# Kernel optimization log

Measured on AMD Instinct MI355X. Metric: run time of the kernel, lower is better.

Reference implementation:

```python
import jax, jax.numpy as jnp
import numpy as np


def setup_inputs() -> dict:
    key = jax.random.key(0)
    # [batch, heads, seq, head_dim]
    hidden_states = jax.random.normal(key, (2, 16, 2048, 64), dtype=jnp.float32)
    return {"hidden_states": hidden_states}


def reference(hidden_states):
    q = k = v = hidden_states
    # scores: [b, h, s, s] -- note: NO 1/sqrt(d) scaling, matching the original.
    scores = jnp.einsum("bhqd,bhkd->bhqk", q, k)
    a = jax.nn.softmax(scores, axis=-1)
    out = jnp.einsum("bhqk,bhkd->bhqd", a, v)
    return out
```

## Files before the change

kernel.cpp:

```cpp
#include <hip/hip_runtime.h>
#include <hip/hip_bf16.h>
#include <stdint.h>


typedef __bf16 bf16x8 __attribute__((ext_vector_type(8)));
typedef __bf16 bf16x4 __attribute__((ext_vector_type(4)));
typedef __bf16 bf16x2 __attribute__((ext_vector_type(2)));
typedef float f32x4 __attribute__((ext_vector_type(4)));
typedef float f32x16 __attribute__((ext_vector_type(16)));
typedef unsigned int u32x4v __attribute__((ext_vector_type(4)));

#define SEQ 2048
#define HD 64
#define KVB 64
#define NBH 32
#define NTILE (SEQ / KVB)
#define IMG_BYTES 8192
#define PAIR_BYTES 16384
#define IMG_TOT ((size_t)NBH * NTILE * PAIR_BYTES)
#define PART_BYTES ((size_t)2 * NBH * SEQ * HD * 4)
#define ML_BYTES ((size_t)2 * NBH * SEQ * 8)
#define WS_IMG IMG_TOT
#define WS_SPLIT (IMG_TOT + PART_BYTES + ML_BYTES)

#define QPB 128

__device__ __forceinline__ int swz(int row, int byteoff) {
    return byteoff ^ ((row & 7) << 4);
}

__device__ __forceinline__ float fexp2(float x) {
    float r;
    asm("v_exp_f32 %0, %1" : "=v"(r) : "v"(x));
    return r;
}

__device__ __forceinline__ unsigned pk_bf16(float a, float b) {
    bf16x2 v;
    v[0] = (__bf16)a;
    v[1] = (__bf16)b;
    return __builtin_bit_cast(unsigned, v);
}

__device__ __forceinline__ bf16x8 read_frag8(const char* base, int r, int p0) {
    const char* rowp = base + r * 128;
    const int rr = r & 15;
    bf16x4 lo = *(const bf16x4*)(rowp + (((p0 + 0) ^ rr) << 3));
    bf16x4 hi4 = *(const bf16x4*)(rowp + (((p0 + 1) ^ rr) << 3));
    bf16x8 f;
    f[0] = lo[0]; f[1] = lo[1]; f[2] = lo[2]; f[3] = lo[3];
    f[4] = hi4[0]; f[5] = hi4[1]; f[6] = hi4[2]; f[7] = hi4[3];
    return f;
}

#if __has_builtin(__builtin_amdgcn_global_load_lds)
#define HAVE_GLLDS 1
typedef const __attribute__((address_space(1))) unsigned int* gas_t;
typedef __attribute__((address_space(3))) unsigned int* las_t;
__device__ __forceinline__ void gl_lds16(const void* g, void* l) {
    __builtin_amdgcn_global_load_lds((gas_t)g, (las_t)l, 16, 0, 0);
}
#else
#define HAVE_GLLDS 0
#endif

__global__ __launch_bounds__(256)
void prep_kernel(const float* __restrict__ x, char* __restrict__ ws) {
    const int bh = blockIdx.y;
    const int tile = blockIdx.x;
    const int kv0 = tile * KVB;
    const int t = threadIdx.x;
    const int srow = t >> 2;
    const int scq = (t & 3) * 16;
    const float* __restrict__ X = x + (size_t)bh * SEQ * HD;
    char* __restrict__ img = ws + ((size_t)bh * NTILE + tile) * PAIR_BYTES;

    const int rr = srow & 15;
    const int p = scq >> 2;

    {
        const float* src = X + (size_t)(kv0 + srow) * HD + scq;
        float4 a = *(const float4*)(src);
        float4 b = *(const float4*)(src + 4);
        float4 c = *(const float4*)(src + 8);
        float4 d = *(const float4*)(src + 12);
        bf16x4 k0, k1, k2, k3;
        k0[0] = (__bf16)a.x; k0[1] = (__bf16)a.y; k0[2] = (__bf16)a.z; k0[3] = (__bf16)a.w;
        k1[0] = (__bf16)b.x; k1[1] = (__bf16)b.y; k1[2] = (__bf16)b.z; k1[3] = (__bf16)b.w;
        k2[0] = (__bf16)c.x; k2[1] = (__bf16)c.y; k2[2] = (__bf16)c.z; k2[3] = (__bf16)c.w;
        k3[0] = (__bf16)d.x; k3[1] = (__bf16)d.y; k3[2] = (__bf16)d.z; k3[3] = (__bf16)d.w;
        char* rowp = img + srow * 128;
        *(bf16x4*)(rowp + (((p + 0) ^ rr) << 3)) = k0;
        *(bf16x4*)(rowp + (((p + 1) ^ rr) << 3)) = k1;
        *(bf16x4*)(rowp + (((p + 2) ^ rr) << 3)) = k2;
        *(bf16x4*)(rowp + (((p + 3) ^ rr) << 3)) = k3;
    }
    {
        bf16x4 g0, g1, g2, g3;
#pragma unroll
        for (int j = 0; j < 4; ++j) {
            g0[j] = (__bf16)X[(size_t)(kv0 + scq + j) * HD + srow];
            g1[j] = (__bf16)X[(size_t)(kv0 + scq + 4 + j) * HD + srow];
            g2[j] = (__bf16)X[(size_t)(kv0 + scq + 8 + j) * HD + srow];
            g3[j] = (__bf16)X[(size_t)(kv0 + scq + 12 + j) * HD + srow];
        }
        char* rowp = img + IMG_BYTES + srow * 128;
        *(bf16x4*)(rowp + (((p + 0) ^ rr) << 3)) = g0;
        *(bf16x4*)(rowp + (((p + 1) ^ rr) << 3)) = g1;
        *(bf16x4*)(rowp + (((p + 2) ^ rr) << 3)) = g2;
        *(bf16x4*)(rowp + (((p + 3) ^ rr) << 3)) = g3;
    }
}

template <int SPLIT>
__global__ __launch_bounds__(256, 4)
void attn_img_kernel(const float* __restrict__ x, const char* __restrict__ ws,
                     float* __restrict__ outp, float* __restrict__ part,
                     float2* __restrict__ ml) {
    __shared__ __align__(16) char kbuf[2][IMG_BYTES];
    __shared__ __align__(16) char vbuf[2][IMG_BYTES];

    const int wg = blockIdx.x;
    const int sid = (wg & 7) * 64 + (wg >> 3);
    const int bh = sid >> 4;
    const int q0 = (sid & 15) * QPB;
    const int half = SPLIT ? blockIdx.y : 0;
    const int tile0 = SPLIT ? half * (NTILE / 2) : 0;
    const int ntiles = SPLIT ? (NTILE / 2) : NTILE;

    const float* __restrict__ X = x + (size_t)bh * SEQ * HD;
    const char* __restrict__ wsb = ws + (size_t)bh * NTILE * PAIR_BYTES;

    const int t = threadIdx.x;
    const int wave = t >> 6;
    const int lane = t & 63;
    const int ln = lane & 31;
    const int hi = lane >> 5;

    const int qbase = q0 + wave * 32;

    const float SCL = 1.4426950408889634f;
    bf16x8 qf[4];
    float m = 0.f;
    {
        const float* qsrc = X + (size_t)(qbase + ln) * HD;
#pragma unroll
        for (int j = 0; j < 16; ++j) {
            float4 v = *(const float4*)(qsrc + j * 4);
            m += v.x * v.x + v.y * v.y + v.z * v.z + v.w * v.w;
        }
        m *= SCL;
#pragma unroll
        for (int dt = 0; dt < 4; ++dt) {
            const float* s8 = qsrc + dt * 16 + hi * 8;
            float4 a = *(const float4*)s8;
            float4 b = *(const float4*)(s8 + 4);
            bf16x8 f;
            f[0] = (__bf16)(a.x * SCL); f[1] = (__bf16)(a.y * SCL);
            f[2] = (__bf16)(a.z * SCL); f[3] = (__bf16)(a.w * SCL);
            f[4] = (__bf16)(b.x * SCL); f[5] = (__bf16)(b.y * SCL);
            f[6] = (__bf16)(b.z * SCL); f[7] = (__bf16)(b.w * SCL);
            qf[dt] = f;
        }
    }

    f32x16 acc0, acc1;
#pragma unroll
    for (int i = 0; i < 16; ++i) { acc0[i] = 0.f; acc1[i] = 0.f; }
    float l = 0.f;

#if HAVE_GLLDS
    {
        char* base = (wave & 2) ? &vbuf[0][(wave & 1) * 4096] : &kbuf[0][(wave & 1) * 4096];
        const char* sp = wsb + (size_t)tile0 * PAIR_BYTES + wave * 4096 + lane * 16;
#pragma unroll
        for (int j = 0; j < 4; ++j)
            gl_lds16(sp + j * 1024, base + j * 1024);
    }
#else
    {
        const char* img = wsb + (size_t)tile0 * PAIR_BYTES;
#pragma unroll
        for (int q = 0; q < 4; ++q) {
            bf16x8 d0 = *(const bf16x8*)(img + q * 4096 + t * 16);
            char* dst = (q & 2) ? &vbuf[0][(q & 1) * 4096] : &kbuf[0][(q & 1) * 4096];
            *(bf16x8*)&dst[t * 16] = d0;
        }
    }
#endif
    __syncthreads();

    for (int it = 0; it < ntiles; ++it) {
        const int cur = it & 1;

#if HAVE_GLLDS
        if (it + 1 < ntiles) {
            const char* img = wsb + (size_t)(tile0 + it + 1) * PAIR_BYTES;
            char* base = (wave & 2) ? &vbuf[cur ^ 1][(wave & 1) * 4096]
                                    : &kbuf[cur ^ 1][(wave & 1) * 4096];
            const char* sp = img + wave * 4096 + lane * 16;
#pragma unroll
            for (int j = 0; j < 4; ++j)
                gl_lds16(sp + j * 1024, base + j * 1024);
        }
#else
        bf16x8 n0, n1, n2, n3;
        if (it + 1 < ntiles) {
            const char* img = wsb + (size_t)(tile0 + it + 1) * PAIR_BYTES;
            n0 = *(const bf16x8*)(img + t * 16);
            n1 = *(const bf16x8*)(img + 4096 + t * 16);
            n2 = *(const bf16x8*)(img + 8192 + t * 16);
            n3 = *(const bf16x8*)(img + 12288 + t * 16);
        }
#endif

        const char* kb = kbuf[cur];
        const char* vb = vbuf[cur];

        f32x16 s0, s1;
#pragma unroll
        for (int i = 0; i < 16; ++i) { s0[i] = 0.f; s1[i] = 0.f; }
        __builtin_amdgcn_s_setprio(1);
#pragma unroll
        for (int dt = 0; dt < 4; ++dt) {
            const int p0 = dt * 4 + hi * 2;
            bf16x8 kf0 = read_frag8(kb, ln, p0);
            s0 = __builtin_amdgcn_mfma_f32_32x32x16_bf16(kf0, qf[dt], s0, 0, 0, 0);
            bf16x8 kf1 = read_frag8(kb, 32 + ln, p0);
            s1 = __builtin_amdgcn_mfma_f32_32x32x16_bf16(kf1, qf[dt], s1, 0, 0, 0);
        }
        __builtin_amdgcn_s_setprio(0);

        f32x16 e0, e1;
#pragma unroll
        for (int i = 0; i < 16; ++i) {
            e0[i] = fexp2(s0[i] - m);
            e1[i] = fexp2(s1[i] - m);
        }
        float ps = 0.f;
#pragma unroll
        for (int i = 0; i < 16; ++i) ps += e0[i] + e1[i];
        ps += __shfl_xor(ps, 32);
        l += ps;

        bf16x8 pa[4];
#pragma unroll
        for (int kt = 0; kt < 4; ++kt) {
            const f32x16& e = (kt & 2) ? e1 : e0;
            const int sx = 8 * (kt & 1);
            unsigned wA = pk_bf16(e[sx + 0], e[sx + 1]);
            unsigned wB = pk_bf16(e[sx + 2], e[sx + 3]);
            unsigned wC = pk_bf16(e[sx + 4], e[sx + 5]);
            unsigned wD = pk_bf16(e[sx + 6], e[sx + 7]);
            asm("v_permlane32_swap_b32 %0, %1" : "+v"(wA), "+v"(wC));
            asm("v_permlane32_swap_b32 %0, %1" : "+v"(wB), "+v"(wD));
            u32x4v w;
            w[0] = wA; w[1] = wB; w[2] = wC; w[3] = wD;
            pa[kt] = __builtin_bit_cast(bf16x8, w);
        }

        __builtin_amdgcn_s_setprio(1);
#pragma unroll
        for (int kt = 0; kt < 4; ++kt) {
            const int p0 = kt * 4 + hi * 2;
            bf16x8 vf0 = read_frag8(vb, ln, p0);
            acc0 = __builtin_amdgcn_mfma_f32_32x32x16_bf16(pa[kt], vf0, acc0, 0, 0, 0);
            bf16x8 vf1 = read_frag8(vb, 32 + ln, p0);
            acc1 = __builtin_amdgcn_mfma_f32_32x32x16_bf16(pa[kt], vf1, acc1, 0, 0, 0);
        }
        __builtin_amdgcn_s_setprio(0);

#if !HAVE_GLLDS
        if (it + 1 < ntiles) {
            const int nxt = cur ^ 1;
            *(bf16x8*)&kbuf[nxt][t * 16] = n0;
            *(bf16x8*)&kbuf[nxt][4096 + t * 16] = n1;
            *(bf16x8*)&vbuf[nxt][t * 16] = n2;
            *(bf16x8*)&vbuf[nxt][4096 + t * 16] = n3;
        }
#endif
        __syncthreads();
    }

    if (SPLIT) {
        float* OP = part + ((size_t)(half * NBH + bh) * SEQ) * HD;
#pragma unroll
        for (int r = 0; r < 16; ++r) {
            const int qr = (r & 3) + 8 * (r >> 2) + 4 * hi;
            float* dst = OP + (size_t)(qbase + qr) * HD + ln;
            dst[0]  = acc0[r];
            dst[32] = acc1[r];
        }
        if (lane < 32)
            ml[(size_t)(half * NBH + bh) * SEQ + qbase + lane] = make_float2(m, l);
    } else {
        float* Op = outp + (size_t)bh * SEQ * HD;
        const float invl = 1.f / l;
#pragma unroll
        for (int r = 0; r < 16; ++r) {
            const int qr = (r & 3) + 8 * (r >> 2) + 4 * hi;
            const float il = __shfl(invl, qr);
            float* dst = Op + (size_t)(qbase + qr) * HD + ln;
            dst[0]  = acc0[r] * il;
            dst[32] = acc1[r] * il;
        }
    }
}

__global__ __launch_bounds__(256)
void merge_kernel(const float* __restrict__ part, const float2* __restrict__ ml,
                  float* __restrict__ outp) {
    const int t = threadIdx.x;
    const size_t row = (size_t)blockIdx.x * 16 + (t >> 4);
    const int c4 = t & 15;
    const size_t NR = (size_t)NBH * SEQ;

    const float2 a = ml[row];
    const float2 b = ml[NR + row];
    const float mN = fmaxf(a.x, b.x);
    const float aA = fexp2(a.x - mN);
    const float aB = fexp2(b.x - mN);
    const float inv = 1.f / (a.y * aA + b.y * aB);

    const f32x4* pA = (const f32x4*)part + row * 16 + c4;
    const f32x4* pB = (const f32x4*)part + (NR + row) * 16 + c4;
    f32x4 va = *pA;
    f32x4 vb = *pB;
    f32x4 o;
#pragma unroll
    for (int j = 0; j < 4; ++j)
        o[j] = (va[j] * aA + vb[j] * aB) * inv;
    *((f32x4*)outp + row * 16 + c4) = o;
}

__global__ __launch_bounds__(256, 2)
void attn_fwd_kernel(const float* __restrict__ x, float* __restrict__ out) {
    __shared__ __align__(16) char k_lds[KVB * HD * 2];
    __shared__ __align__(16) char vt_lds[HD * KVB * 2];
    __shared__ __align__(16) char p_lds2[4][2][16 * KVB * 2];

    const int bh = blockIdx.y;
    const int q0 = blockIdx.x * 128;
    const float* __restrict__ X = x + (size_t)bh * SEQ * HD;
    float* __restrict__ Op = out + (size_t)bh * SEQ * HD;

    const int t = threadIdx.x;
    const int wave = t >> 6;
    const int lane = t & 63;
    const int lgrp = lane >> 4;
    const int lid = lane & 15;

    bf16x8 qf[2][2];
#pragma unroll
    for (int rt = 0; rt < 2; ++rt) {
        const int row = q0 + wave * 32 + rt * 16 + lid;
#pragma unroll
        for (int kc = 0; kc < 2; ++kc) {
            const float* src = X + (size_t)row * HD + kc * 32 + lgrp * 8;
            float4 a = *(const float4*)src;
            float4 b = *(const float4*)(src + 4);
            bf16x8 f;
            f[0] = (__bf16)a.x; f[1] = (__bf16)a.y; f[2] = (__bf16)a.z; f[3] = (__bf16)a.w;
            f[4] = (__bf16)b.x; f[5] = (__bf16)b.y; f[6] = (__bf16)b.z; f[7] = (__bf16)b.w;
            qf[rt][kc] = f;
        }
    }

    f32x4 acc[2][4];
    float m[2][4], l[2][4];
#pragma unroll
    for (int rt = 0; rt < 2; ++rt)
#pragma unroll
        for (int i = 0; i < 4; ++i) {
            acc[rt][i][0] = 0.f; acc[rt][i][1] = 0.f;
            acc[rt][i][2] = 0.f; acc[rt][i][3] = 0.f;
            m[rt][i] = -1e30f;
            l[rt][i] = 0.f;
        }

    const int srow = t >> 2;
    const int scq = (t & 3) * 16;

    for (int kv0 = 0; kv0 < SEQ; kv0 += KVB) {
        {
            const float* src = X + (size_t)(kv0 + srow) * HD + scq;
            float4 a = *(const float4*)(src);
            float4 b = *(const float4*)(src + 4);
            float4 c = *(const float4*)(src + 8);
            float4 d = *(const float4*)(src + 12);
            bf16x8 f0, f1;
            f0[0] = (__bf16)a.x; f0[1] = (__bf16)a.y; f0[2] = (__bf16)a.z; f0[3] = (__bf16)a.w;
            f0[4] = (__bf16)b.x; f0[5] = (__bf16)b.y; f0[6] = (__bf16)b.z; f0[7] = (__bf16)b.w;
            f1[0] = (__bf16)c.x; f1[1] = (__bf16)c.y; f1[2] = (__bf16)c.z; f1[3] = (__bf16)c.w;
            f1[4] = (__bf16)d.x; f1[5] = (__bf16)d.y; f1[6] = (__bf16)d.z; f1[7] = (__bf16)d.w;
            *(bf16x8*)&k_lds[swz(srow, srow * 128 + scq * 2)] = f0;
            *(bf16x8*)&k_lds[swz(srow, srow * 128 + scq * 2 + 16)] = f1;
        }
        {
            bf16x8 g0, g1;
#pragma unroll
            for (int j = 0; j < 8; ++j)
                g0[j] = (__bf16)X[(size_t)(kv0 + scq + j) * HD + srow];
#pragma unroll
            for (int j = 0; j < 8; ++j)
                g1[j] = (__bf16)X[(size_t)(kv0 + scq + 8 + j) * HD + srow];
            *(bf16x8*)&vt_lds[swz(srow, srow * 128 + scq * 2)] = g0;
            *(bf16x8*)&vt_lds[swz(srow, srow * 128 + scq * 2 + 16)] = g1;
        }
        __syncthreads();

#pragma unroll
        for (int rt = 0; rt < 2; ++rt) {
            f32x4 s[4];
#pragma unroll
            for (int kt = 0; kt < 4; ++kt) {
                f32x4 z = {0.f, 0.f, 0.f, 0.f};
#pragma unroll
                for (int kc = 0; kc < 2; ++kc) {
                    const int krow = kt * 16 + lid;
                    bf16x8 kfr = *(const bf16x8*)&k_lds[swz(krow, krow * 128 + (kc * 32 + lgrp * 8) * 2)];
                    z = __builtin_amdgcn_mfma_f32_16x16x32_bf16(qf[rt][kc], kfr, z, 0, 0, 0);
                }
                s[kt] = z;
            }

            char* pl = p_lds2[wave][rt];
#pragma unroll
            for (int r = 0; r < 4; ++r) {
                float mxv = fmaxf(fmaxf(s[0][r], s[1][r]), fmaxf(s[2][r], s[3][r]));
                mxv = fmaxf(mxv, __shfl_xor(mxv, 1));
                mxv = fmaxf(mxv, __shfl_xor(mxv, 2));
                mxv = fmaxf(mxv, __shfl_xor(mxv, 4));
                mxv = fmaxf(mxv, __shfl_xor(mxv, 8));
                const float mold = m[rt][r];
                const float mnew = fmaxf(mold, mxv);
                const float alpha = __expf(mold - mnew);
                const int prow = lgrp * 4 + r;
                float psum = 0.f;
#pragma unroll
                for (int kt = 0; kt < 4; ++kt) {
                    float p = __expf(s[kt][r] - mnew);
                    psum += p;
                    *(__bf16*)&pl[swz(prow, prow * 128 + (kt * 16 + lid) * 2)] = (__bf16)p;
                }
                psum += __shfl_xor(psum, 1);
                psum += __shfl_xor(psum, 2);
                psum += __shfl_xor(psum, 4);
                psum += __shfl_xor(psum, 8);
                l[rt][r] = l[rt][r] * alpha + psum;
                m[rt][r] = mnew;
#pragma unroll
                for (int ct = 0; ct < 4; ++ct)
                    acc[rt][ct][r] *= alpha;
            }

#pragma unroll
            for (int kc = 0; kc < 2; ++kc) {
                bf16x8 pfr = *(const bf16x8*)&pl[swz(lid, lid * 128 + (kc * 32 + lgrp * 8) * 2)];
#pragma unroll
                for (int ct = 0; ct < 4; ++ct) {
                    const int vrow = ct * 16 + lid;
                    bf16x8 vf = *(const bf16x8*)&vt_lds[swz(vrow, vrow * 128 + (kc * 32 + lgrp * 8) * 2)];
                    acc[rt][ct] = __builtin_amdgcn_mfma_f32_16x16x32_bf16(pfr, vf, acc[rt][ct], 0, 0, 0);
                }
            }
        }
        __syncthreads();
    }

#pragma unroll
    for (int rt = 0; rt < 2; ++rt)
#pragma unroll
        for (int r = 0; r < 4; ++r) {
            const float inv = 1.f / l[rt][r];
            const int row = q0 + wave * 32 + rt * 16 + lgrp * 4 + r;
            float* dst = Op + (size_t)row * HD + lid;
#pragma unroll
            for (int ct = 0; ct < 4; ++ct)
                dst[ct * 16] = acc[rt][ct][r] * inv;
        }
}

extern "C" void kernel_launch(void* const* d_in, const int* in_sizes, int n_in,
                              void* d_out, int out_size, void* d_ws, size_t ws_size,
                              hipStream_t stream) {
    const float* x = (const float*)d_in[0];
    float* out = (float*)d_out;
    char* ws = (char*)d_ws;
    if (ws_size >= WS_SPLIT) {
        float* part = (float*)(ws + IMG_TOT);
        float2* ml = (float2*)(ws + IMG_TOT + PART_BYTES);
        dim3 pgrid(NTILE, NBH);
        hipLaunchKernelGGL(prep_kernel, pgrid, dim3(256), 0, stream, x, ws);
        hipLaunchKernelGGL((attn_img_kernel<1>), dim3(512, 2), dim3(256), 0, stream,
                           x, ws, out, part, ml);
        hipLaunchKernelGGL(merge_kernel, dim3(NBH * SEQ / 16), dim3(256), 0, stream,
                           part, ml, out);
    } else if (ws_size >= WS_IMG) {
        dim3 pgrid(NTILE, NBH);
        hipLaunchKernelGGL(prep_kernel, pgrid, dim3(256), 0, stream, x, ws);
        hipLaunchKernelGGL((attn_img_kernel<0>), dim3(512, 1), dim3(256), 0, stream,
                           x, ws, out, nullptr, nullptr);
    } else {
        dim3 grid(SEQ / 128, NBH);
        hipLaunchKernelGGL(attn_fwd_kernel, grid, dim3(256), 0, stream, x, out);
    }
}
```

Before: 76.54 us.

## Drop split-KV merge, compute row sums via MFMA with ones, fold max into accumulator init

Removes the two-way KV split and the separate merge kernel, so each workgroup covers all KV tiles and writes normalized output directly. The softmax row sum is now built by an extra MFMA of P against a bf16 ones vector, replacing the VALU reduction and cross-lane shuffle. The fixed max offset is folded into the score accumulator's initial value, removing a subtraction per element. This halves the grid to 512 workgroups, which may lower occupancy and parallelism on the device. The row sum now comes from bf16-rounded probabilities rather than fp32 values.

```diff
diff --git a/kernel.cpp b/kernel.cpp
--- a/kernel.cpp
+++ b/kernel.cpp
@@ -18,10 +18,7 @@
 #define IMG_BYTES 8192
 #define PAIR_BYTES 16384
 #define IMG_TOT ((size_t)NBH * NTILE * PAIR_BYTES)
-#define PART_BYTES ((size_t)2 * NBH * SEQ * HD * 4)
-#define ML_BYTES ((size_t)2 * NBH * SEQ * 8)
 #define WS_IMG IMG_TOT
-#define WS_SPLIT (IMG_TOT + PART_BYTES + ML_BYTES)
 
 #define QPB 128
 
@@ -112,11 +109,9 @@
     }
 }
 
-template <int SPLIT>
 __global__ __launch_bounds__(256, 4)
 void attn_img_kernel(const float* __restrict__ x, const char* __restrict__ ws,
-                     float* __restrict__ outp, float* __restrict__ part,
-                     float2* __restrict__ ml) {
+                     float* __restrict__ outp) {
     __shared__ __align__(16) char kbuf[2][IMG_BYTES];
     __shared__ __align__(16) char vbuf[2][IMG_BYTES];
 
@@ -124,9 +119,6 @@
     const int sid = (wg & 7) * 64 + (wg >> 3);
     const int bh = sid >> 4;
     const int q0 = (sid & 15) * QPB;
-    const int half = SPLIT ? blockIdx.y : 0;
-    const int tile0 = SPLIT ? half * (NTILE / 2) : 0;
-    const int ntiles = SPLIT ? (NTILE / 2) : NTILE;
 
     const float* __restrict__ X = x + (size_t)bh * SEQ * HD;
     const char* __restrict__ wsb = ws + (size_t)bh * NTILE * PAIR_BYTES;
@@ -163,23 +155,30 @@
             qf[dt] = f;
         }
     }
-
-    f32x16 acc0, acc1;
-#pragma unroll
-    for (int i = 0; i < 16; ++i) { acc0[i] = 0.f; acc1[i] = 0.f; }
-    float l = 0.f;
+    const float negm = -m;
+
+    bf16x8 onef;
+    {
+        u32x4v w;
+        w[0] = 0x3F803F80u; w[1] = 0x3F803F80u; w[2] = 0x3F803F80u; w[3] = 0x3F803F80u;
+        onef = __builtin_bit_cast(bf16x8, w);
+    }
+
+    f32x16 acc0, acc1, lac;
+#pragma unroll
+    for (int i = 0; i < 16; ++i) { acc0[i] = 0.f; acc1[i] = 0.f; lac[i] = 0.f; }
 
 #if HAVE_GLLDS
     {
         char* base = (wave & 2) ? &vbuf[0][(wave & 1) * 4096] : &kbuf[0][(wave & 1) * 4096];
-        const char* sp = wsb + (size_t)tile0 * PAIR_BYTES + wave * 4096 + lane * 16;
+        const char* sp = wsb + wave * 4096 + lane * 16;
 #pragma unroll
         for (int j = 0; j < 4; ++j)
             gl_lds16(sp + j * 1024, base + j * 1024);
     }
 #else
     {
-        const char* img = wsb + (size_t)tile0 * PAIR_BYTES;
+        const char* img = wsb;
 #pragma unroll
         for (int q = 0; q < 4; ++q) {
             bf16x8 d0 = *(const bf16x8*)(img + q * 4096 + t * 16);
@@ -190,12 +189,12 @@
 #endif
     __syncthreads();
 
-    for (int it = 0; it < ntiles; ++it) {
+    for (int it = 0; it < NTILE; ++it) {
         const int cur = it & 1;
 
 #if HAVE_GLLDS
-        if (it + 1 < ntiles) {
-            const char* img = wsb + (size_t)(tile0 + it + 1) * PAIR_BYTES;
+        if (it + 1 < NTILE) {
+            const char* img = wsb + (size_t)(it + 1) * PAIR_BYTES;
             char* base = (wave & 2) ? &vbuf[cur ^ 1][(wave & 1) * 4096]
                                     : &kbuf[cur ^ 1][(wave & 1) * 4096];
             const char* sp = img + wave * 4096 + lane * 16;
@@ -205,8 +204,8 @@
         }
 #else
         bf16x8 n0, n1, n2, n3;
-        if (it + 1 < ntiles) {
-            const char* img = wsb + (size_t)(tile0 + it + 1) * PAIR_BYTES;
+        if (it + 1 < NTILE) {
+            const char* img = wsb + (size_t)(it + 1) * PAIR_BYTES;
             n0 = *(const bf16x8*)(img + t * 16);
             n1 = *(const bf16x8*)(img + 4096 + t * 16);
             n2 = *(const bf16x8*)(img + 8192 + t * 16);
@@ -219,7 +218,7 @@
 
         f32x16 s0, s1;
 #pragma unroll
-        for (int i = 0; i < 16; ++i) { s0[i] = 0.f; s1[i] = 0.f; }
+        for (int i = 0; i < 16; ++i) { s0[i] = negm; s1[i] = negm; }
         __builtin_amdgcn_s_setprio(1);
 #pragma unroll
         for (int dt = 0; dt < 4; ++dt) {
@@ -234,14 +233,9 @@
         f32x16 e0, e1;
 #pragma unroll
         for (int i = 0; i < 16; ++i) {
-            e0[i] = fexp2(s0[i] - m);
-            e1[i] = fexp2(s1[i] - m);
-        }
-        float ps = 0.f;
-#pragma unroll
-        for (int i = 0; i < 16; ++i) ps += e0[i] + e1[i];
-        ps += __shfl_xor(ps, 32);
-        l += ps;
+            e0[i] = fexp2(s0[i]);
+            e1[i] = fexp2(s1[i]);
+        }
 
         bf16x8 pa[4];
 #pragma unroll
@@ -267,11 +261,12 @@
             acc0 = __builtin_amdgcn_mfma_f32_32x32x16_bf16(pa[kt], vf0, acc0, 0, 0, 0);
             bf16x8 vf1 = read_frag8(vb, 32 + ln, p0);
             acc1 = __builtin_amdgcn_mfma_f32_32x32x16_bf16(pa[kt], vf1, acc1, 0, 0, 0);
+            lac = __builtin_amdgcn_mfma_f32_32x32x16_bf16(pa[kt], onef, lac, 0, 0, 0);
         }
         __builtin_amdgcn_s_setprio(0);
 
 #if !HAVE_GLLDS
-        if (it + 1 < ntiles) {
+        if (it + 1 < NTILE) {
             const int nxt = cur ^ 1;
             *(bf16x8*)&kbuf[nxt][t * 16] = n0;
             *(bf16x8*)&kbuf[nxt][4096 + t * 16] = n1;
@@ -282,55 +277,15 @@
         __syncthreads();
     }
 
-    if (SPLIT) {
-        float* OP = part + ((size_t)(half * NBH + bh) * SEQ) * HD;
-#pragma unroll
-        for (int r = 0; r < 16; ++r) {
-            const int qr = (r & 3) + 8 * (r >> 2) + 4 * hi;
-            float* dst = OP + (size_t)(qbase + qr) * HD + ln;
-            dst[0]  = acc0[r];
-            dst[32] = acc1[r];
-        }
-        if (lane < 32)
-            ml[(size_t)(half * NBH + bh) * SEQ + qbase + lane] = make_float2(m, l);
-    } else {
-        float* Op = outp + (size_t)bh * SEQ * HD;
-        const float invl = 1.f / l;
-#pragma unroll
-        for (int r = 0; r < 16; ++r) {
-            const int qr = (r & 3) + 8 * (r >> 2) + 4 * hi;
-            const float il = __shfl(invl, qr);
-            float* dst = Op + (size_t)(qbase + qr) * HD + ln;
-            dst[0]  = acc0[r] * il;
-            dst[32] = acc1[r] * il;
-        }
-    }
-}
-
-__global__ __launch_bounds__(256)
-void merge_kernel(const float* __restrict__ part, const float2* __restrict__ ml,
-                  float* __restrict__ outp) {
-    const int t = threadIdx.x;
-    const size_t row = (size_t)blockIdx.x * 16 + (t >> 4);
-    const int c4 = t & 15;
-    const size_t NR = (size_t)NBH * SEQ;
-
-    const float2 a = ml[row];
-    const float2 b = ml[NR + row];
-    const float mN = fmaxf(a.x, b.x);
-    const float aA = fexp2(a.x - mN);
-    const float aB = fexp2(b.x - mN);
-    const float inv = 1.f / (a.y * aA + b.y * aB);
-
-    const f32x4* pA = (const f32x4*)part + row * 16 + c4;
-    const f32x4* pB = (const f32x4*)part + (NR + row) * 16 + c4;
-    f32x4 va = *pA;
-    f32x4 vb = *pB;
-    f32x4 o;
-#pragma unroll
-    for (int j = 0; j < 4; ++j)
-        o[j] = (va[j] * aA + vb[j] * aB) * inv;
-    *((f32x4*)outp + row * 16 + c4) = o;
+    float* Op = outp + (size_t)bh * SEQ * HD;
+#pragma unroll
+    for (int r = 0; r < 16; ++r) {
+        const int qr = (r & 3) + 8 * (r >> 2) + 4 * hi;
+        const float il = 1.f / lac[r];
+        float* dst = Op + (size_t)(qbase + qr) * HD + ln;
+        dst[0]  = acc0[r] * il;
+        dst[32] = acc1[r] * il;
+    }
 }
 
 __global__ __launch_bounds__(256, 2)
@@ -487,20 +442,11 @@
     const float* x = (const float*)d_in[0];
     float* out = (float*)d_out;
     char* ws = (char*)d_ws;
-    if (ws_size >= WS_SPLIT) {
-        float* part = (float*)(ws + IMG_TOT);
-        float2* ml = (float2*)(ws + IMG_TOT + PART_BYTES);
+    if (ws_size >= WS_IMG) {
         dim3 pgrid(NTILE, NBH);
         hipLaunchKernelGGL(prep_kernel, pgrid, dim3(256), 0, stream, x, ws);
-        hipLaunchKernelGGL((attn_img_kernel<1>), dim3(512, 2), dim3(256), 0, stream,
-                           x, ws, out, part, ml);
-        hipLaunchKernelGGL(merge_kernel, dim3(NBH * SEQ / 16), dim3(256), 0, stream,
-                           part, ml, out);
-    } else if (ws_size >= WS_IMG) {
-        dim3 pgrid(NTILE, NBH);
-        hipLaunchKernelGGL(prep_kernel, pgrid, dim3(256), 0, stream, x, ws);
-        hipLaunchKernelGGL((attn_img_kernel<0>), dim3(512, 1), dim3(256), 0, stream,
-                           x, ws, out, nullptr, nullptr);
+        hipLaunchKernelGGL(attn_img_kernel, dim3(512), dim3(256), 0, stream,
+                           x, ws, out);
     } else {
         dim3 grid(SEQ / 128, NBH);
         hipLaunchKernelGGL(attn_fwd_kernel, grid, dim3(256), 0, stream, x, out);
```

Result: slower. 85.63 us (+11.9%).
